# Kernel optimization log

Hardware: AMD Instinct MI355X
Metric: run time of the kernel (lower is better)

Reference implementation:

```python
import jax, jax.numpy as jnp
import numpy as np

B, SEQ, D, H, PRED = 131072, 150, 2, 64, 150


def setup_inputs() -> dict:
    key = jax.random.key(0)
    ks = jax.random.split(key, 5)
    s1 = 1.0 / np.sqrt(D)  # torch Linear default init bounds
    s2 = 1.0 / np.sqrt(H)
    return {
        "x": jax.random.normal(ks[0], (B, SEQ, D), jnp.float32),
        "W1": jax.random.uniform(ks[1], (D, H), jnp.float32, -s1, s1),
        "b1": jax.random.uniform(ks[2], (H,), jnp.float32, -s1, s1),
        "W2": jax.random.uniform(ks[3], (H, D), jnp.float32, -s2, s2),
        "b2": jax.random.uniform(ks[4], (D,), jnp.float32, -s2, s2),
    }


def reference(x, W1, b1, W2, b2):
    # ODE RHS: autonomous 2-layer MLP, f(t, y) = tanh(y W1 + b1) W2 + b2
    def f(y):
        return jnp.tanh(y @ W1 + b1) @ W2 + b2

    y0 = x[:, -1, :]  # [B, D]
    t = jnp.linspace(0.0, float(PRED), PRED)  # 150 grid points -> 149 steps
    dts = t[1:] - t[:-1]  # each = 150/149

    # torchdiffeq method='rk4' uses the 3/8-rule fixed-grid step (rk4_alt_step_func)
    def step(y, dt):
        k1 = f(y)
        k2 = f(y + dt * k1 / 3.0)
        k3 = f(y + dt * (k2 - k1 / 3.0))
        k4 = f(y + dt * (k1 - k2 + k3))
        y1 = y + dt * (k1 + 3.0 * (k2 + k3) + k4) / 8.0
        return y1, y1

    _, ys = jax.lax.scan(step, y0, dts)  # ys: [PRED-1, B, D]
    pred = jnp.concatenate([y0[None], ys], axis=0)  # [PRED, B, D]
    return pred.transpose(1, 0, 2)  # [B, PRED, D]
```

## Files before the change

kernel.cpp:

```cpp
#include <hip/hip_runtime.h>

#ifndef __has_builtin
#define __has_builtin(x) 0
#endif

__device__ __forceinline__ float fast_exp2(float x) {
#if __has_builtin(__builtin_amdgcn_exp2f)
  return __builtin_amdgcn_exp2f(x);
#else
  return exp2f(x);
#endif
}
__device__ __forceinline__ float fast_rcp(float x) {
#if __has_builtin(__builtin_amdgcn_rcpf)
  return __builtin_amdgcn_rcpf(x);
#else
  return 1.0f / x;
#endif
}

namespace {
constexpr int kB = 131072;
constexpr int kSeq = 150;
constexpr int kD = 2;
constexpr int kH = 64;
constexpr int kPred = 150;
constexpr int kSteps = kPred - 1;
constexpr float kDt = 150.0f / 149.0f;
constexpr float kC = 2.8853900817779268f;
constexpr int kSplit = 4;
constexpr int kHper = kH / kSplit;
constexpr int kBlock = 256;
constexpr int kElemsPerBlock = kBlock / kSplit;
}

__device__ __forceinline__ float dpp_xor1_add(float v) {
  int s = __builtin_amdgcn_update_dpp(0, __float_as_int(v), 0xB1, 0xF, 0xF, true);
  return v + __int_as_float(s);
}
__device__ __forceinline__ float dpp_xor2_add(float v) {
  int s = __builtin_amdgcn_update_dpp(0, __float_as_int(v), 0x4E, 0xF, 0xF, true);
  return v + __int_as_float(s);
}

__global__ __launch_bounds__(kBlock, 4) void ode_kernel(
    const float* __restrict__ x, const float* __restrict__ W1,
    const float* __restrict__ b1, const float* __restrict__ W2,
    const float* __restrict__ b2, float* __restrict__ out) {
  const int t = threadIdx.x;
  const int part = t & (kSplit - 1);
  const int j0 = part * kHper;

  float wx[kHper], wy[kHper], wz[kHper], ww[kHper], wb[kHper];
#pragma unroll
  for (int i = 0; i < kHper; ++i) {
    const int j = j0 + i;
    wx[i] = W1[j] * kC;
    wy[i] = W1[kH + j] * kC;
    wb[i] = b1[j] * kC;
    wz[i] = -2.0f * W2[2 * j];
    ww[i] = -2.0f * W2[2 * j + 1];
  }
  float pb0 = 0.25f * b2[0];
  float pb1 = 0.25f * b2[1];
#pragma unroll
  for (int i = 0; i < kHper; ++i) {
    pb0 = fmaf(-0.5f, wz[i], pb0);
    pb1 = fmaf(-0.5f, ww[i], pb1);
  }

  const long elem = (long)blockIdx.x * kElemsPerBlock + (t >> 2);
  const float* xp = x + elem * (long)(kSeq * kD) + (kSeq - 1) * kD;
  float y0 = xp[0];
  float y1 = xp[1];
  float* op = out + elem * (long)(kPred * kD);

  auto feval = [&](float u0, float u1, float& f0, float& f1) {
    float a0 = pb0, a1 = pb1, c0 = 0.0f, c1 = 0.0f;
#pragma unroll
    for (int i = 0; i < kHper; i += 2) {
      float p0 = fmaf(u0, wx[i], fmaf(u1, wy[i], wb[i]));
      float r0 = fast_rcp(1.0f + fast_exp2(p0));
      a0 = fmaf(r0, wz[i], a0);
      a1 = fmaf(r0, ww[i], a1);
      float p1 = fmaf(u0, wx[i + 1], fmaf(u1, wy[i + 1], wb[i + 1]));
      float r1 = fast_rcp(1.0f + fast_exp2(p1));
      c0 = fmaf(r1, wz[i + 1], c0);
      c1 = fmaf(r1, ww[i + 1], c1);
    }
    a0 += c0;
    a1 += c1;
    a0 = dpp_xor2_add(dpp_xor1_add(a0));
    a1 = dpp_xor2_add(dpp_xor1_add(a1));
    f0 = a0;
    f1 = a1;
  };

  float py0 = y0, py1 = y1;
  constexpr float DT = kDt, DT3 = kDt / 3.0f, DT8 = kDt / 8.0f;

  for (int s = 1; s <= kSteps; ++s) {
    float k1x, k1y, k2x, k2y, k3x, k3y, k4x, k4y;
    feval(y0, y1, k1x, k1y);
    feval(fmaf(DT3, k1x, y0), fmaf(DT3, k1y, y1), k2x, k2y);
    feval(fmaf(DT, k2x, fmaf(-DT3, k1x, y0)),
          fmaf(DT, k2y, fmaf(-DT3, k1y, y1)), k3x, k3y);
    feval(fmaf(DT, k1x - k2x + k3x, y0),
          fmaf(DT, k1y - k2y + k3y, y1), k4x, k4y);
    y0 = fmaf(DT8, k1x + 3.0f * (k2x + k3x) + k4x, y0);
    y1 = fmaf(DT8, k1y + 3.0f * (k2y + k3y) + k4y, y1);

    if (s & 1) {
      if (part == 0) {
        float4 v = make_float4(py0, py1, y0, y1);
        *reinterpret_cast<float4*>(op + (long)(s - 1) * 2) = v;
      }
    } else {
      py0 = y0;
      py1 = y1;
    }
  }
}

extern "C" void kernel_launch(void* const* d_in, const int* in_sizes, int n_in,
                              void* d_out, int out_size, void* d_ws,
                              size_t ws_size, hipStream_t stream) {
  const float* x = (const float*)d_in[0];
  const float* W1 = (const float*)d_in[1];
  const float* b1 = (const float*)d_in[2];
  const float* W2 = (const float*)d_in[3];
  const float* b2 = (const float*)d_in[4];
  float* out = (float*)d_out;

  dim3 grid(kB * kSplit / kBlock);
  dim3 block(kBlock);
  hipLaunchKernelGGL(ode_kernel, grid, block, 0, stream, x, W1, b1, W2, b2,
                     out);
}
```

Baseline: 1.350 ms.

## Pack MLP evaluation into float2 ops and share one reciprocal across four sigmoids

```diff
diff --git a/kernel.cpp b/kernel.cpp
--- a/kernel.cpp
+++ b/kernel.cpp
@@ -3,6 +3,8 @@
 #ifndef __has_builtin
 #define __has_builtin(x) 0
 #endif
+
+typedef float v2 __attribute__((ext_vector_type(2)));
 
 __device__ __forceinline__ float fast_exp2(float x) {
 #if __has_builtin(__builtin_amdgcn_exp2f)
@@ -19,6 +21,10 @@
 #endif
 }
 
+__device__ __forceinline__ v2 vfma(v2 a, v2 b, v2 c) {
+  return __builtin_elementwise_fma(a, b, c);
+}
+
 namespace {
 constexpr int kB = 131072;
 constexpr int kSeq = 150;
@@ -28,22 +34,24 @@
 constexpr int kSteps = kPred - 1;
 constexpr float kDt = 150.0f / 149.0f;
 constexpr float kC = 2.8853900817779268f;
+constexpr float kClamp = 30.0f;
 constexpr int kSplit = 4;
 constexpr int kHper = kH / kSplit;
 constexpr int kBlock = 256;
 constexpr int kElemsPerBlock = kBlock / kSplit;
 }
 
-__device__ __forceinline__ float dpp_xor1_add(float v) {
-  int s = __builtin_amdgcn_update_dpp(0, __float_as_int(v), 0xB1, 0xF, 0xF, true);
-  return v + __int_as_float(s);
-}
-__device__ __forceinline__ float dpp_xor2_add(float v) {
-  int s = __builtin_amdgcn_update_dpp(0, __float_as_int(v), 0x4E, 0xF, 0xF, true);
-  return v + __int_as_float(s);
+template <int PAT>
+__device__ __forceinline__ v2 dpp_swap(v2 v) {
+  int lo = __builtin_amdgcn_update_dpp(0, __float_as_int(v.x), PAT, 0xF, 0xF, true);
+  int hi = __builtin_amdgcn_update_dpp(0, __float_as_int(v.y), PAT, 0xF, 0xF, true);
+  v2 r;
+  r.x = __int_as_float(lo);
+  r.y = __int_as_float(hi);
+  return r;
 }
 
-__global__ __launch_bounds__(kBlock, 4) void ode_kernel(
+__global__ __launch_bounds__(kBlock, 3) void ode_kernel(
     const float* __restrict__ x, const float* __restrict__ W1,
     const float* __restrict__ b1, const float* __restrict__ W2,
     const float* __restrict__ b2, float* __restrict__ out) {
@@ -51,73 +59,97 @@
   const int part = t & (kSplit - 1);
   const int j0 = part * kHper;
 
-  float wx[kHper], wy[kHper], wz[kHper], ww[kHper], wb[kHper];
+  v2 wx[kHper / 2], wy[kHper / 2], wb[kHper / 2], wz[kHper / 2], ww[kHper / 2];
 #pragma unroll
-  for (int i = 0; i < kHper; ++i) {
-    const int j = j0 + i;
-    wx[i] = W1[j] * kC;
-    wy[i] = W1[kH + j] * kC;
-    wb[i] = b1[j] * kC;
-    wz[i] = -2.0f * W2[2 * j];
-    ww[i] = -2.0f * W2[2 * j + 1];
+  for (int i = 0; i < kHper / 2; ++i) {
+    const int j = j0 + 2 * i;
+    wx[i].x = W1[j] * kC;
+    wx[i].y = W1[j + 1] * kC;
+    wy[i].x = W1[kH + j] * kC;
+    wy[i].y = W1[kH + j + 1] * kC;
+    wb[i].x = b1[j] * kC;
+    wb[i].y = b1[j + 1] * kC;
+    wz[i].x = -2.0f * W2[2 * j];
+    wz[i].y = -2.0f * W2[2 * (j + 1)];
+    ww[i].x = -2.0f * W2[2 * j + 1];
+    ww[i].y = -2.0f * W2[2 * (j + 1) + 1];
   }
-  float pb0 = 0.25f * b2[0];
-  float pb1 = 0.25f * b2[1];
+  v2 pb;
+  pb.x = 0.25f * b2[0];
+  pb.y = 0.25f * b2[1];
 #pragma unroll
-  for (int i = 0; i < kHper; ++i) {
-    pb0 = fmaf(-0.5f, wz[i], pb0);
-    pb1 = fmaf(-0.5f, ww[i], pb1);
+  for (int i = 0; i < kHper / 2; ++i) {
+    pb.x = fmaf(-0.5f, wz[i].x + wz[i].y, pb.x);
+    pb.y = fmaf(-0.5f, ww[i].x + ww[i].y, pb.y);
   }
 
   const long elem = (long)blockIdx.x * kElemsPerBlock + (t >> 2);
   const float* xp = x + elem * (long)(kSeq * kD) + (kSeq - 1) * kD;
-  float y0 = xp[0];
-  float y1 = xp[1];
+  v2 y = *reinterpret_cast<const v2*>(xp);
   float* op = out + elem * (long)(kPred * kD);
 
-  auto feval = [&](float u0, float u1, float& f0, float& f1) {
-    float a0 = pb0, a1 = pb1, c0 = 0.0f, c1 = 0.0f;
+  auto feval = [&](v2 u) -> v2 {
+    v2 acc0a, acc1a, acc0b, acc1b;
+    acc0a.x = pb.x; acc0a.y = 0.0f;
+    acc1a.x = pb.y; acc1a.y = 0.0f;
+    acc0b.x = 0.0f; acc0b.y = 0.0f;
+    acc1b.x = 0.0f; acc1b.y = 0.0f;
+    v2 U0, U1;
+    U0.x = u.x; U0.y = u.x;
+    U1.x = u.y; U1.y = u.y;
 #pragma unroll
-    for (int i = 0; i < kHper; i += 2) {
-      float p0 = fmaf(u0, wx[i], fmaf(u1, wy[i], wb[i]));
-      float r0 = fast_rcp(1.0f + fast_exp2(p0));
-      a0 = fmaf(r0, wz[i], a0);
-      a1 = fmaf(r0, ww[i], a1);
-      float p1 = fmaf(u0, wx[i + 1], fmaf(u1, wy[i + 1], wb[i + 1]));
-      float r1 = fast_rcp(1.0f + fast_exp2(p1));
-      c0 = fmaf(r1, wz[i + 1], c0);
-      c1 = fmaf(r1, ww[i + 1], c1);
+    for (int g = 0; g < kHper / 4; ++g) {
+      const int iA = 2 * g, iB = 2 * g + 1;
+      v2 pA = vfma(U0, wx[iA], vfma(U1, wy[iA], wb[iA]));
+      v2 pB = vfma(U0, wx[iB], vfma(U1, wy[iB], wb[iB]));
+      pA = __builtin_elementwise_min(pA, (v2)kClamp);
+      pB = __builtin_elementwise_min(pB, (v2)kClamp);
+      v2 eA, eB;
+      eA.x = fast_exp2(pA.x);
+      eA.y = fast_exp2(pA.y);
+      eB.x = fast_exp2(pB.x);
+      eB.y = fast_exp2(pB.y);
+      v2 sA = eA + 1.0f;
+      v2 sB = eB + 1.0f;
+      float mA = sA.x * sA.y;
+      float mB = sB.x * sB.y;
+      float R = fast_rcp(mA * mB);
+      float tA = mB * R;
+      float tB = mA * R;
+      v2 rA = sA.yx * tA;
+      v2 rB = sB.yx * tB;
+      acc0a = vfma(rA, wz[iA], acc0a);
+      acc1a = vfma(rA, ww[iA], acc1a);
+      acc0b = vfma(rB, wz[iB], acc0b);
+      acc1b = vfma(rB, ww[iB], acc1b);
     }
-    a0 += c0;
-    a1 += c1;
-    a0 = dpp_xor2_add(dpp_xor1_add(a0));
-    a1 = dpp_xor2_add(dpp_xor1_add(a1));
-    f0 = a0;
-    f1 = a1;
+    v2 s0 = acc0a + acc0b;
+    v2 s1 = acc1a + acc1b;
+    v2 f;
+    f.x = s0.x + s0.y;
+    f.y = s1.x + s1.y;
+    f = f + dpp_swap<0xB1>(f);
+    f = f + dpp_swap<0x4E>(f);
+    return f;
   };
 
-  float py0 = y0, py1 = y1;
+  v2 py = y;
   constexpr float DT = kDt, DT3 = kDt / 3.0f, DT8 = kDt / 8.0f;
 
   for (int s = 1; s <= kSteps; ++s) {
-    float k1x, k1y, k2x, k2y, k3x, k3y, k4x, k4y;
-    feval(y0, y1, k1x, k1y);
-    feval(fmaf(DT3, k1x, y0), fmaf(DT3, k1y, y1), k2x, k2y);
-    feval(fmaf(DT, k2x, fmaf(-DT3, k1x, y0)),
-          fmaf(DT, k2y, fmaf(-DT3, k1y, y1)), k3x, k3y);
-    feval(fmaf(DT, k1x - k2x + k3x, y0),
-          fmaf(DT, k1y - k2y + k3y, y1), k4x, k4y);
-    y0 = fmaf(DT8, k1x + 3.0f * (k2x + k3x) + k4x, y0);
-    y1 = fmaf(DT8, k1y + 3.0f * (k2y + k3y) + k4y, y1);
+    v2 k1 = feval(y);
+    v2 k2 = feval(vfma((v2)DT3, k1, y));
+    v2 k3 = feval(vfma((v2)DT, k2, vfma((v2)(-DT3), k1, y)));
+    v2 k4 = feval(vfma((v2)DT, (k1 - k2) + k3, y));
+    y = vfma((v2)DT8, vfma((v2)3.0f, k2 + k3, k1) + k4, y);
 
     if (s & 1) {
       if (part == 0) {
-        float4 v = make_float4(py0, py1, y0, y1);
+        float4 v = make_float4(py.x, py.y, y.x, y.y);
         *reinterpret_cast<float4*>(op + (long)(s - 1) * 2) = v;
       }
     } else {
-      py0 = y0;
-      py1 = y1;
+      py = y;
     }
   }
 }
```

Result: slower. 1.444 ms (+6.9%).

## Use packed FP32 FMAs and a shared reciprocal across four sigmoids

Applied to the files above, without the earlier changes.

```diff
diff --git a/kernel.cpp b/kernel.cpp
--- a/kernel.cpp
+++ b/kernel.cpp
@@ -3,6 +3,8 @@
 #ifndef __has_builtin
 #define __has_builtin(x) 0
 #endif
+
+typedef float v2 __attribute__((ext_vector_type(2)));
 
 __device__ __forceinline__ float fast_exp2(float x) {
 #if __has_builtin(__builtin_amdgcn_exp2f)
@@ -28,22 +30,21 @@
 constexpr int kSteps = kPred - 1;
 constexpr float kDt = 150.0f / 149.0f;
 constexpr float kC = 2.8853900817779268f;
+constexpr float kClamp = 30.0f;
 constexpr int kSplit = 4;
 constexpr int kHper = kH / kSplit;
+constexpr int kPairs = kHper / 2;
 constexpr int kBlock = 256;
 constexpr int kElemsPerBlock = kBlock / kSplit;
 }
 
-__device__ __forceinline__ float dpp_xor1_add(float v) {
-  int s = __builtin_amdgcn_update_dpp(0, __float_as_int(v), 0xB1, 0xF, 0xF, true);
-  return v + __int_as_float(s);
-}
-__device__ __forceinline__ float dpp_xor2_add(float v) {
-  int s = __builtin_amdgcn_update_dpp(0, __float_as_int(v), 0x4E, 0xF, 0xF, true);
+template <int PAT>
+__device__ __forceinline__ float dpp_add(float v) {
+  int s = __builtin_amdgcn_update_dpp(0, __float_as_int(v), PAT, 0xF, 0xF, true);
   return v + __int_as_float(s);
 }
 
-__global__ __launch_bounds__(kBlock, 4) void ode_kernel(
+__global__ __launch_bounds__(kBlock, 3) void ode_kernel(
     const float* __restrict__ x, const float* __restrict__ W1,
     const float* __restrict__ b1, const float* __restrict__ W2,
     const float* __restrict__ b2, float* __restrict__ out) {
@@ -51,73 +52,112 @@
   const int part = t & (kSplit - 1);
   const int j0 = part * kHper;
 
-  float wx[kHper], wy[kHper], wz[kHper], ww[kHper], wb[kHper];
+  v2 wx[kPairs], wy[kPairs], wb[kPairs], wz[kPairs], ww[kPairs];
+  {
+    const v2* w1r0 = reinterpret_cast<const v2*>(W1 + j0);
+    const v2* w1r1 = reinterpret_cast<const v2*>(W1 + kH + j0);
+    const v2* b1p = reinterpret_cast<const v2*>(b1 + j0);
 #pragma unroll
-  for (int i = 0; i < kHper; ++i) {
-    const int j = j0 + i;
-    wx[i] = W1[j] * kC;
-    wy[i] = W1[kH + j] * kC;
-    wb[i] = b1[j] * kC;
-    wz[i] = -2.0f * W2[2 * j];
-    ww[i] = -2.0f * W2[2 * j + 1];
+    for (int i = 0; i < kPairs; ++i) {
+      wx[i] = w1r0[i] * kC;
+      wy[i] = w1r1[i] * kC;
+      wb[i] = b1p[i] * kC;
+      const int j = j0 + 2 * i;
+      wz[i].x = -2.0f * W2[2 * j];
+      wz[i].y = -2.0f * W2[2 * (j + 1)];
+      ww[i].x = -2.0f * W2[2 * j + 1];
+      ww[i].y = -2.0f * W2[2 * (j + 1) + 1];
+    }
   }
   float pb0 = 0.25f * b2[0];
   float pb1 = 0.25f * b2[1];
 #pragma unroll
-  for (int i = 0; i < kHper; ++i) {
-    pb0 = fmaf(-0.5f, wz[i], pb0);
-    pb1 = fmaf(-0.5f, ww[i], pb1);
+  for (int i = 0; i < kPairs; ++i) {
+    pb0 = fmaf(-0.5f, wz[i].x + wz[i].y, pb0);
+    pb1 = fmaf(-0.5f, ww[i].x + ww[i].y, pb1);
+  }
+#pragma unroll
+  for (int i = 0; i < kPairs; ++i) {
+    asm volatile("" : "+v"(wx[i]), "+v"(wy[i]), "+v"(wb[i]), "+v"(wz[i]),
+                      "+v"(ww[i]));
   }
 
   const long elem = (long)blockIdx.x * kElemsPerBlock + (t >> 2);
   const float* xp = x + elem * (long)(kSeq * kD) + (kSeq - 1) * kD;
-  float y0 = xp[0];
-  float y1 = xp[1];
+  v2 y = *reinterpret_cast<const v2*>(xp);
   float* op = out + elem * (long)(kPred * kD);
 
-  auto feval = [&](float u0, float u1, float& f0, float& f1) {
-    float a0 = pb0, a1 = pb1, c0 = 0.0f, c1 = 0.0f;
-#pragma unroll
-    for (int i = 0; i < kHper; i += 2) {
-      float p0 = fmaf(u0, wx[i], fmaf(u1, wy[i], wb[i]));
-      float r0 = fast_rcp(1.0f + fast_exp2(p0));
-      a0 = fmaf(r0, wz[i], a0);
-      a1 = fmaf(r0, ww[i], a1);
-      float p1 = fmaf(u0, wx[i + 1], fmaf(u1, wy[i + 1], wb[i + 1]));
-      float r1 = fast_rcp(1.0f + fast_exp2(p1));
-      c0 = fmaf(r1, wz[i + 1], c0);
-      c1 = fmaf(r1, ww[i + 1], c1);
-    }
-    a0 += c0;
-    a1 += c1;
-    a0 = dpp_xor2_add(dpp_xor1_add(a0));
-    a1 = dpp_xor2_add(dpp_xor1_add(a1));
-    f0 = a0;
-    f1 = a1;
+  auto feval = [&](v2 u) -> v2 {
+    v2 accA0, accA1, accB0, accB1;
+#define GRP(iA, iB, FIRST)                                                    \
+  {                                                                           \
+    v2 pA, pB;                                                                \
+    asm("v_pk_fma_f32 %0, %1, %2, %3 op_sel:[1,0,0] op_sel_hi:[1,1,1]"        \
+        : "=v"(pA) : "v"(u), "v"(wy[iA]), "v"(wb[iA]));                       \
+    asm("v_pk_fma_f32 %0, %1, %2, %0 op_sel:[0,0,0] op_sel_hi:[0,1,1]"        \
+        : "+v"(pA) : "v"(u), "v"(wx[iA]));                                    \
+    asm("v_pk_fma_f32 %0, %1, %2, %3 op_sel:[1,0,0] op_sel_hi:[1,1,1]"        \
+        : "=v"(pB) : "v"(u), "v"(wy[iB]), "v"(wb[iB]));                       \
+    asm("v_pk_fma_f32 %0, %1, %2, %0 op_sel:[0,0,0] op_sel_hi:[0,1,1]"        \
+        : "+v"(pB) : "v"(u), "v"(wx[iB]));                                    \
+    float s0 = 1.0f + fast_exp2(fminf(pA.x, kClamp));                         \
+    float s1 = 1.0f + fast_exp2(fminf(pA.y, kClamp));                         \
+    float s2 = 1.0f + fast_exp2(fminf(pB.x, kClamp));                         \
+    float s3 = 1.0f + fast_exp2(fminf(pB.y, kClamp));                         \
+    float m01 = s0 * s1, m23 = s2 * s3;                                       \
+    float R = fast_rcp(m01 * m23);                                            \
+    float t01 = m23 * R, t23 = m01 * R;                                       \
+    v2 rA, rB;                                                                \
+    rA.x = s1 * t01;                                                          \
+    rA.y = s0 * t01;                                                          \
+    rB.x = s3 * t23;                                                          \
+    rB.y = s2 * t23;                                                          \
+    if (FIRST) {                                                              \
+      asm("v_pk_mul_f32 %0, %1, %2" : "=v"(accA0) : "v"(rA), "v"(wz[iA]));    \
+      asm("v_pk_mul_f32 %0, %1, %2" : "=v"(accA1) : "v"(rA), "v"(ww[iA]));    \
+      asm("v_pk_mul_f32 %0, %1, %2" : "=v"(accB0) : "v"(rB), "v"(wz[iB]));    \
+      asm("v_pk_mul_f32 %0, %1, %2" : "=v"(accB1) : "v"(rB), "v"(ww[iB]));    \
+    } else {                                                                  \
+      asm("v_pk_fma_f32 %0, %1, %2, %0" : "+v"(accA0) : "v"(rA), "v"(wz[iA]));\
+      asm("v_pk_fma_f32 %0, %1, %2, %0" : "+v"(accA1) : "v"(rA), "v"(ww[iA]));\
+      asm("v_pk_fma_f32 %0, %1, %2, %0" : "+v"(accB0) : "v"(rB), "v"(wz[iB]));\
+      asm("v_pk_fma_f32 %0, %1, %2, %0" : "+v"(accB1) : "v"(rB), "v"(ww[iB]));\
+    }                                                                         \
+  }
+    GRP(0, 1, true)
+    GRP(2, 3, false)
+    GRP(4, 5, false)
+    GRP(6, 7, false)
+#undef GRP
+    v2 a0 = accA0 + accB0;
+    v2 a1 = accA1 + accB1;
+    v2 f;
+    f.x = pb0 + a0.x + a0.y;
+    f.y = pb1 + a1.x + a1.y;
+    f.x = dpp_add<0x4E>(dpp_add<0xB1>(f.x));
+    f.y = dpp_add<0x4E>(dpp_add<0xB1>(f.y));
+    return f;
   };
 
-  float py0 = y0, py1 = y1;
+  v2 py = y;
   constexpr float DT = kDt, DT3 = kDt / 3.0f, DT8 = kDt / 8.0f;
 
   for (int s = 1; s <= kSteps; ++s) {
-    float k1x, k1y, k2x, k2y, k3x, k3y, k4x, k4y;
-    feval(y0, y1, k1x, k1y);
-    feval(fmaf(DT3, k1x, y0), fmaf(DT3, k1y, y1), k2x, k2y);
-    feval(fmaf(DT, k2x, fmaf(-DT3, k1x, y0)),
-          fmaf(DT, k2y, fmaf(-DT3, k1y, y1)), k3x, k3y);
-    feval(fmaf(DT, k1x - k2x + k3x, y0),
-          fmaf(DT, k1y - k2y + k3y, y1), k4x, k4y);
-    y0 = fmaf(DT8, k1x + 3.0f * (k2x + k3x) + k4x, y0);
-    y1 = fmaf(DT8, k1y + 3.0f * (k2y + k3y) + k4y, y1);
+    v2 k1 = feval(y);
+    v2 k2 = feval(__builtin_elementwise_fma((v2)DT3, k1, y));
+    v2 k3 = feval(__builtin_elementwise_fma(
+        (v2)DT, k2, __builtin_elementwise_fma((v2)(-DT3), k1, y)));
+    v2 k4 = feval(__builtin_elementwise_fma((v2)DT, (k1 - k2) + k3, y));
+    y = __builtin_elementwise_fma(
+        (v2)DT8, __builtin_elementwise_fma((v2)3.0f, k2 + k3, k1) + k4, y);
 
     if (s & 1) {
       if (part == 0) {
-        float4 v = make_float4(py0, py1, y0, y1);
+        float4 v = make_float4(py.x, py.y, y.x, y.y);
         *reinterpret_cast<float4*>(op + (long)(s - 1) * 2) = v;
       }
     } else {
-      py0 = y0;
-      py1 = y1;
+      py = y;
     }
   }
 }
```

Measured after the change: 1.571 ms. 16.4% more time.

## Split hidden units over 8 lanes and batch reciprocals via product trick

Applied to the files above, without the earlier changes.

```diff
diff --git a/kernel.cpp b/kernel.cpp
--- a/kernel.cpp
+++ b/kernel.cpp
@@ -3,6 +3,8 @@
 #ifndef __has_builtin
 #define __has_builtin(x) 0
 #endif
+
+typedef float v2 __attribute__((ext_vector_type(2)));
 
 __device__ __forceinline__ float fast_exp2(float x) {
 #if __has_builtin(__builtin_amdgcn_exp2f)
@@ -28,18 +30,16 @@
 constexpr int kSteps = kPred - 1;
 constexpr float kDt = 150.0f / 149.0f;
 constexpr float kC = 2.8853900817779268f;
-constexpr int kSplit = 4;
+constexpr float kClamp = 30.0f;
+constexpr int kSplit = 8;
 constexpr int kHper = kH / kSplit;
 constexpr int kBlock = 256;
 constexpr int kElemsPerBlock = kBlock / kSplit;
 }
 
-__device__ __forceinline__ float dpp_xor1_add(float v) {
-  int s = __builtin_amdgcn_update_dpp(0, __float_as_int(v), 0xB1, 0xF, 0xF, true);
-  return v + __int_as_float(s);
-}
-__device__ __forceinline__ float dpp_xor2_add(float v) {
-  int s = __builtin_amdgcn_update_dpp(0, __float_as_int(v), 0x4E, 0xF, 0xF, true);
+template <int PAT>
+__device__ __forceinline__ float dpp_add(float v) {
+  int s = __builtin_amdgcn_update_dpp(0, __float_as_int(v), PAT, 0xF, 0xF, true);
   return v + __int_as_float(s);
 }
 
@@ -51,7 +51,7 @@
   const int part = t & (kSplit - 1);
   const int j0 = part * kHper;
 
-  float wx[kHper], wy[kHper], wz[kHper], ww[kHper], wb[kHper];
+  float wx[kHper], wy[kHper], wb[kHper], wz[kHper], ww[kHper];
 #pragma unroll
   for (int i = 0; i < kHper; ++i) {
     const int j = j0 + i;
@@ -61,41 +61,76 @@
     wz[i] = -2.0f * W2[2 * j];
     ww[i] = -2.0f * W2[2 * j + 1];
   }
-  float pb0 = 0.25f * b2[0];
-  float pb1 = 0.25f * b2[1];
+  float pb0 = 0.125f * b2[0];
+  float pb1 = 0.125f * b2[1];
 #pragma unroll
   for (int i = 0; i < kHper; ++i) {
     pb0 = fmaf(-0.5f, wz[i], pb0);
     pb1 = fmaf(-0.5f, ww[i], pb1);
   }
+#pragma unroll
+  for (int i = 0; i < kHper; ++i) {
+    asm volatile("" : "+v"(wx[i]), "+v"(wy[i]), "+v"(wb[i]), "+v"(wz[i]),
+                      "+v"(ww[i]));
+  }
 
-  const long elem = (long)blockIdx.x * kElemsPerBlock + (t >> 2);
+  const long elem = (long)blockIdx.x * kElemsPerBlock + (t >> 3);
   const float* xp = x + elem * (long)(kSeq * kD) + (kSeq - 1) * kD;
-  float y0 = xp[0];
-  float y1 = xp[1];
+  v2 y = *reinterpret_cast<const v2*>(xp);
   float* op = out + elem * (long)(kPred * kD);
 
   auto feval = [&](float u0, float u1, float& f0, float& f1) {
-    float a0 = pb0, a1 = pb1, c0 = 0.0f, c1 = 0.0f;
-#pragma unroll
-    for (int i = 0; i < kHper; i += 2) {
-      float p0 = fmaf(u0, wx[i], fmaf(u1, wy[i], wb[i]));
-      float r0 = fast_rcp(1.0f + fast_exp2(p0));
-      a0 = fmaf(r0, wz[i], a0);
-      a1 = fmaf(r0, ww[i], a1);
-      float p1 = fmaf(u0, wx[i + 1], fmaf(u1, wy[i + 1], wb[i + 1]));
-      float r1 = fast_rcp(1.0f + fast_exp2(p1));
-      c0 = fmaf(r1, wz[i + 1], c0);
-      c1 = fmaf(r1, ww[i + 1], c1);
-    }
-    a0 += c0;
-    a1 += c1;
-    a0 = dpp_xor2_add(dpp_xor1_add(a0));
-    a1 = dpp_xor2_add(dpp_xor1_add(a1));
-    f0 = a0;
-    f1 = a1;
+    float pA0 = fminf(fmaf(u0, wx[0], fmaf(u1, wy[0], wb[0])), kClamp);
+    float pA1 = fminf(fmaf(u0, wx[1], fmaf(u1, wy[1], wb[1])), kClamp);
+    float pA2 = fminf(fmaf(u0, wx[2], fmaf(u1, wy[2], wb[2])), kClamp);
+    float pA3 = fminf(fmaf(u0, wx[3], fmaf(u1, wy[3], wb[3])), kClamp);
+    float pB0 = fminf(fmaf(u0, wx[4], fmaf(u1, wy[4], wb[4])), kClamp);
+    float pB1 = fminf(fmaf(u0, wx[5], fmaf(u1, wy[5], wb[5])), kClamp);
+    float pB2 = fminf(fmaf(u0, wx[6], fmaf(u1, wy[6], wb[6])), kClamp);
+    float pB3 = fminf(fmaf(u0, wx[7], fmaf(u1, wy[7], wb[7])), kClamp);
+    float sA0 = 1.0f + fast_exp2(pA0);
+    float sA1 = 1.0f + fast_exp2(pA1);
+    float sA2 = 1.0f + fast_exp2(pA2);
+    float sA3 = 1.0f + fast_exp2(pA3);
+    float sB0 = 1.0f + fast_exp2(pB0);
+    float sB1 = 1.0f + fast_exp2(pB1);
+    float sB2 = 1.0f + fast_exp2(pB2);
+    float sB3 = 1.0f + fast_exp2(pB3);
+    float mA01 = sA0 * sA1, mA23 = sA2 * sA3;
+    float mB01 = sB0 * sB1, mB23 = sB2 * sB3;
+    float RA = fast_rcp(mA01 * mA23);
+    float RB = fast_rcp(mB01 * mB23);
+    float tA01 = mA23 * RA, tA23 = mA01 * RA;
+    float tB01 = mB23 * RB, tB23 = mB01 * RB;
+    float rA0 = sA1 * tA01, rA1 = sA0 * tA01;
+    float rA2 = sA3 * tA23, rA3 = sA2 * tA23;
+    float rB0 = sB1 * tB01, rB1 = sB0 * tB01;
+    float rB2 = sB3 * tB23, rB3 = sB2 * tB23;
+    float a0 = fmaf(rA0, wz[0], pb0);
+    float a1 = fmaf(rA0, ww[0], pb1);
+    float c0 = rB0 * wz[4];
+    float c1 = rB0 * ww[4];
+    a0 = fmaf(rA1, wz[1], a0);
+    a1 = fmaf(rA1, ww[1], a1);
+    c0 = fmaf(rB1, wz[5], c0);
+    c1 = fmaf(rB1, ww[5], c1);
+    a0 = fmaf(rA2, wz[2], a0);
+    a1 = fmaf(rA2, ww[2], a1);
+    c0 = fmaf(rB2, wz[6], c0);
+    c1 = fmaf(rB2, ww[6], c1);
+    a0 = fmaf(rA3, wz[3], a0);
+    a1 = fmaf(rA3, ww[3], a1);
+    c0 = fmaf(rB3, wz[7], c0);
+    c1 = fmaf(rB3, ww[7], c1);
+    float fx = a0 + c0;
+    float fy = a1 + c1;
+    fx = dpp_add<0x141>(dpp_add<0x4E>(dpp_add<0xB1>(fx)));
+    fy = dpp_add<0x141>(dpp_add<0x4E>(dpp_add<0xB1>(fy)));
+    f0 = fx;
+    f1 = fy;
   };
 
+  float y0 = y.x, y1 = y.y;
   float py0 = y0, py1 = y1;
   constexpr float DT = kDt, DT3 = kDt / 3.0f, DT8 = kDt / 8.0f;
 
```

Measured after the change: 1.639 ms. +21.4%, slower.
